# Kernel optimization log

Hardware: AMD Instinct MI355X
Metric: run time of the kernel (lower is better)

The kernel has to match this reference:

```python
import jax, jax.numpy as jnp
from jax import lax
import numpy as np

N = 8000                      # number of input points (also padded unique-voxel count)
PC_RANGE = (-50.0, -50.0, -3.0, 50.0, 50.0, 3.0)
VOXEL = (0.25, 0.25, 6.0)     # cluster_voxel_size
CONN_DIST = 0.6               # connected_dist
GX = int(np.floor((PC_RANGE[3] - PC_RANGE[0]) / VOXEL[0])) + 1
GY = int(np.floor((PC_RANGE[4] - PC_RANGE[1]) / VOXEL[1])) + 1
GZ = int(np.floor((PC_RANGE[5] - PC_RANGE[2]) / VOXEL[2])) + 1


def setup_inputs() -> dict:
    key = jax.random.key(0)
    u = jax.random.uniform(key, (N, 3), dtype=jnp.float32)
    lo = jnp.array(PC_RANGE[:3], jnp.float32)
    hi = jnp.array(PC_RANGE[3:], jnp.float32)
    points = lo + u * (hi - lo)          # points spread over the full pc_range
    batch_idx = jnp.zeros((N,), jnp.int32)  # single batch (eval path)
    return {"points": points, "batch_idx": batch_idx}


def _voxel_ids(points, batch_idx):
    lo = jnp.array(PC_RANGE[:3], dtype=points.dtype)
    vs = jnp.array(VOXEL, dtype=points.dtype)
    coors = jnp.floor((points - lo) / vs).astype(jnp.int32)
    coors = jnp.clip(coors, 0, jnp.array([GX - 1, GY - 1, GZ - 1], jnp.int32))
    # linearize (batch, cx, cy, cz) -> single int id (equivalent to unique over rows)
    return ((batch_idx * GX + coors[:, 0]) * GY + coors[:, 1]) * GZ + coors[:, 2]


def reference(points, batch_idx):
    # ---- scatter_v2(mode='avg'): voxelize + per-voxel mean ----
    vid = _voxel_ids(points, batch_idx)
    _, inv = jnp.unique(vid, size=N, fill_value=-1, return_inverse=True)
    inv = inv.reshape(-1)
    ones = jnp.ones((N,), points.dtype)
    counts = jax.ops.segment_sum(ones, inv, num_segments=N)           # [N]
    centers = jax.ops.segment_sum(points, inv, num_segments=N) / jnp.maximum(counts, 1.0)[:, None]
    valid = counts > 0                                                # real (non-padded) voxels

    # ---- radius adjacency over xy of voxel centers ----
    xy = centers[:, :2]
    sq = jnp.sum(xy * xy, axis=1)
    d2 = sq[:, None] + sq[None, :] - 2.0 * (xy @ xy.T)
    dmat = jnp.sqrt(jnp.maximum(d2, 0.0))                             # [N,N]
    pair_valid = valid[:, None] & valid[None, :]
    adj = (jnp.where(pair_valid, dmat, jnp.inf) < CONN_DIST) | jnp.eye(N, dtype=bool)

    # ---- connected components via min-label propagation + pointer jumping ----
    labels0 = jnp.arange(N, dtype=jnp.int32)

    def body_fn(state):
        l, _ = state
        nl = jnp.min(jnp.where(adj, l[None, :], N), axis=1).astype(jnp.int32)
        nl = jnp.minimum(nl, nl[nl])  # pointer jump accelerates convergence
        return (nl, jnp.all(nl == l))

    labels, _ = lax.while_loop(lambda st: jnp.logical_not(st[1]), body_fn, (labels0, jnp.array(False)))

    # compress component roots to dense 0..K-1 in first-occurrence order
    # (scipy.connected_components labels components by min node index order);
    # padded slots are pushed after all real components.
    comp_key = jnp.where(valid, labels, labels + N)
    _, comp = jnp.unique(comp_key, size=N, fill_value=2 * N, return_inverse=True)
    comp = comp.reshape(-1).astype(jnp.int32)

    cluster_inds = comp[inv]                                          # per-point component id
    cls = jnp.zeros((N,), jnp.int32)                                  # modify_cluster_by_class, class 0
    cluster_inds_per_point = jnp.stack([cls, batch_idx, cluster_inds], axis=1)  # [N,3]
    valid_mask = jnp.ones((N,), bool)                                 # min_points=1 -> all kept
    return cluster_inds_per_point, valid_mask
```

## Files before the change

kernel.cpp:

```cpp
#include <hip/hip_runtime.h>
#include <math.h>
#include <limits.h>

#define NPTS   8000
#define GXD    401
#define GYD    401
#define GZD    2
#define MVOX   321602
#define TS     256
#define NTB    32
#define NPAIR  528

__global__ void k_vid(const float* __restrict__ pts, const int* __restrict__ batch,
                      int* __restrict__ vid, int* __restrict__ V,
                      int* __restrict__ inv, float* __restrict__ cnt,
                      float* __restrict__ sx, float* __restrict__ sy) {
  int p = blockIdx.x * blockDim.x + threadIdx.x;
  if (p >= NPTS) return;
  inv[p] = 0; cnt[p] = 0.0f; sx[p] = 0.0f; sy[p] = 0.0f;
  float x = pts[3 * p + 0], y = pts[3 * p + 1], z = pts[3 * p + 2];
  int cx = (int)floorf((x + 50.0f) / 0.25f);
  int cy = (int)floorf((y + 50.0f) / 0.25f);
  int cz = (int)floorf((z + 3.0f) / 6.0f);
  cx = min(max(cx, 0), GXD - 1);
  cy = min(max(cy, 0), GYD - 1);
  cz = min(max(cz, 0), GZD - 1);
  int b = batch[p];
  int v = ((b * GXD + cx) * GYD + cy) * GZD + cz;
  v = min(max(v, 0), MVOX - 1);
  vid[p] = v;
  atomicMin(&V[v], p);
}

__global__ void k_rank(const int* __restrict__ vid, const int* __restrict__ V,
                       int* __restrict__ inv) {
  __shared__ alignas(16) int rs[TS];
  int t = threadIdx.x;
  int j = blockIdx.y * TS + t;
  int r = INT_MAX;
  if (j < NPTS) {
    int vv = vid[j];
    r = (V[vv] == j) ? vv : INT_MAX;
  }
  rs[t] = r;
  __syncthreads();
  int p = blockIdx.x * TS + t;
  if (p >= NPTS) return;
  int v = vid[p];
  int c = 0;
  const int4* rs4 = (const int4*)rs;
  #pragma unroll 16
  for (int k4 = 0; k4 < TS / 4; ++k4) {
    int4 q = rs4[k4];
    c += (q.x < v) ? 1 : 0;
    c += (q.y < v) ? 1 : 0;
    c += (q.z < v) ? 1 : 0;
    c += (q.w < v) ? 1 : 0;
  }
  if (c) atomicAdd(&inv[p], c);
}

__global__ void k_accum(const float* __restrict__ pts, const int* __restrict__ inv,
                        float* __restrict__ cnt, float* __restrict__ sx,
                        float* __restrict__ sy, int* __restrict__ parent) {
  int p = blockIdx.x * blockDim.x + threadIdx.x;
  if (p >= NPTS) return;
  parent[p] = p;
  int s = inv[p];
  atomicAdd(&cnt[s], 1.0f);
  atomicAdd(&sx[s], pts[3 * p + 0]);
  atomicAdd(&sy[s], pts[3 * p + 1]);
}

__device__ __forceinline__ int load_par(int* parent, int x) {
  return __hip_atomic_load(&parent[x], __ATOMIC_RELAXED, __HIP_MEMORY_SCOPE_AGENT);
}

__device__ void hook(int* parent, int u, int v) {
  int ru = u, rv = v;
  while (true) {
    int p;
    while ((p = load_par(parent, ru)) != ru) ru = p;
    while ((p = load_par(parent, rv)) != rv) rv = p;
    if (ru == rv) return;
    int hi = ru > rv ? ru : rv;
    int lo = ru ^ rv ^ hi;
    int old = atomicCAS(&parent[hi], hi, lo);
    if (old == hi) return;
    ru = lo; rv = old;
  }
}

__device__ __forceinline__ float4 center_of(int u, const float* cnt,
                                            const float* sx, const float* sy) {
  float c = cnt[u];
  float d = fmaxf(c, 1.0f);
  float X = sx[u] / d;
  float Y = sy[u] / d;
  float sq = (c > 0.0f) ? (X * X + Y * Y) : 1e30f;
  return make_float4(X, Y, sq, 0.0f);
}

__global__ void k_edges(const float* __restrict__ cnt, const float* __restrict__ sx,
                        const float* __restrict__ sy, int* __restrict__ parent) {
  __shared__ float4 tile[TS];
  int t = threadIdx.x;
  int e = blockIdx.x;
  int by = (int)((sqrtf(8.0f * (float)e + 1.0f) - 1.0f) * 0.5f);
  while ((by + 1) * (by + 2) / 2 <= e) ++by;
  while (by * (by + 1) / 2 > e) --by;
  int bx = e - by * (by + 1) / 2;
  int j0 = by * TS;
  int j = j0 + t;
  tile[t] = (j < NPTS) ? center_of(j, cnt, sx, sy)
                       : make_float4(0.0f, 0.0f, 1e30f, 0.0f);
  __syncthreads();
  int i = bx * TS + t;
  if (i >= NPTS) return;
  float4 qi = center_of(i, cnt, sx, sy);
  float xi = qi.x, yi = qi.y, si = qi.z;
  for (int kb = 0; kb < TS; kb += 64) {
    unsigned long long m = 0;
    #pragma unroll
    for (int k2 = 0; k2 < 64; ++k2) {
      float4 q = tile[kb + k2];
      float d2 = si + q.z - 2.0f * (xi * q.x + yi * q.y);
      if (d2 < 0.36f) m |= (1ull << k2);
    }
    while (m) {
      int k2 = __ffsll(m) - 1;
      m &= m - 1;
      hook(parent, i, j0 + kb + k2);
    }
  }
}

__global__ void k_post(int* __restrict__ parent, const float* __restrict__ cnt,
                       int* __restrict__ labels, int* __restrict__ compRank) {
  int t = threadIdx.x;
  int b = blockIdx.x;
  if (b == 0) {
    __shared__ int sc[TS];
    unsigned flags = 0;
    int base = t * 32;
    int s = 0;
    #pragma unroll
    for (int k = 0; k < 32; ++k) {
      int i = base + k;
      int fl = 0;
      if (i < NPTS) fl = (cnt[i] > 0.0f && parent[i] == i) ? 1 : 0;
      flags |= (unsigned)fl << k;
      s += fl;
    }
    sc[t] = s;
    __syncthreads();
    for (int off = 1; off < TS; off <<= 1) {
      int v = sc[t];
      int a = (t >= off) ? sc[t - off] : 0;
      __syncthreads();
      sc[t] = v + a;
      __syncthreads();
    }
    int excl = sc[t] - s;
    #pragma unroll
    for (int k = 0; k < 32; ++k) {
      int i = base + k;
      if (i < NPTS) { compRank[i] = excl; excl += (flags >> k) & 1; }
    }
  } else {
    int u = (b - 1) * TS + t;
    if (u < NPTS) {
      int x = u, p;
      while ((p = parent[x]) != x) x = p;
      labels[u] = x;
    }
  }
}

__global__ void k_out(const int* __restrict__ inv, const int* __restrict__ labels,
                      const int* __restrict__ compRank, const int* __restrict__ batch,
                      int* __restrict__ out) {
  int p = blockIdx.x * blockDim.x + threadIdx.x;
  if (p >= NPTS) return;
  int lab = labels[inv[p]];
  out[3 * p + 0] = 0;
  out[3 * p + 1] = batch[p];
  out[3 * p + 2] = compRank[lab];
  out[3 * NPTS + p] = 1;
}

extern "C" void kernel_launch(void* const* d_in, const int* in_sizes, int n_in,
                              void* d_out, int out_size, void* d_ws, size_t ws_size,
                              hipStream_t stream) {
  const float* pts   = (const float*)d_in[0];
  const int*   batch = (const int*)d_in[1];
  int* outp = (int*)d_out;

  char* base = (char*)d_ws;
  size_t o = 0;
  int*   V       = (int*)(base + o);   o += ((size_t)MVOX * 4 + 255) & ~(size_t)255;
  int*   vid     = (int*)(base + o);   o += NPTS * 4;
  int*   inv     = (int*)(base + o);   o += NPTS * 4;
  float* cnt     = (float*)(base + o); o += NPTS * 4;
  float* sx      = (float*)(base + o); o += NPTS * 4;
  float* sy      = (float*)(base + o); o += NPTS * 4;
  int*   parent  = (int*)(base + o);   o += NPTS * 4;
  int*   labels  = (int*)(base + o);   o += NPTS * 4;
  int*   compRank= (int*)(base + o);   o += NPTS * 4;

  hipMemsetAsync(V, 0x7F, (size_t)MVOX * 4, stream);

  dim3 b256(TS);
  k_vid  <<<dim3(NTB),       b256, 0, stream>>>(pts, batch, vid, V, inv, cnt, sx, sy);
  k_rank <<<dim3(NTB, NTB),  b256, 0, stream>>>(vid, V, inv);
  k_accum<<<dim3(NTB),       b256, 0, stream>>>(pts, inv, cnt, sx, sy, parent);
  k_edges<<<dim3(NPAIR),     b256, 0, stream>>>(cnt, sx, sy, parent);
  k_post <<<dim3(NTB + 1),   b256, 0, stream>>>(parent, cnt, labels, compRank);
  k_out  <<<dim3(NTB),       b256, 0, stream>>>(inv, labels, compRank, batch, outp);
}
```

Before: 105.9 us.

## Replace unique/rank pipeline with per-block shared-memory voxel bitmap and fused post-processing

Voxel uniqueness and ranking now come from a shared-memory occupancy bitmap plus a popcount prefix scan, computed redundantly in each of 32 blocks. This removes the 1.3MB memset, the atomicMin table and the O(N^2/256) rank kernel. Each block accumulates the per-voxel sums for its own 250-slot segment in shared memory, so no global atomics are needed. The post and out kernels are merged: each output block recomputes the root-flag scan and finds roots inline. This cuts the launch count from 7 to 3, at the cost of redundant per-block scans and a serial popcount loop over bitmap words for each point.

```diff
diff --git a/kernel.cpp b/kernel.cpp
--- a/kernel.cpp
+++ b/kernel.cpp
@@ -7,17 +7,15 @@
 #define GYD    401
 #define GZD    2
 #define MVOX   321602
+#define NW     10051
+#define NCH    252
 #define TS     256
 #define NTB    32
 #define NPAIR  528
-
-__global__ void k_vid(const float* __restrict__ pts, const int* __restrict__ batch,
-                      int* __restrict__ vid, int* __restrict__ V,
-                      int* __restrict__ inv, float* __restrict__ cnt,
-                      float* __restrict__ sx, float* __restrict__ sy) {
-  int p = blockIdx.x * blockDim.x + threadIdx.x;
-  if (p >= NPTS) return;
-  inv[p] = 0; cnt[p] = 0.0f; sx[p] = 0.0f; sy[p] = 0.0f;
+#define SEGB   250
+
+__device__ __forceinline__ int vox_of(const float* __restrict__ pts,
+                                      const int* __restrict__ batch, int p) {
   float x = pts[3 * p + 0], y = pts[3 * p + 1], z = pts[3 * p + 2];
   int cx = (int)floorf((x + 50.0f) / 0.25f);
   int cy = (int)floorf((y + 50.0f) / 0.25f);
@@ -27,49 +25,63 @@
   cz = min(max(cz, 0), GZD - 1);
   int b = batch[p];
   int v = ((b * GXD + cx) * GYD + cy) * GZD + cz;
-  v = min(max(v, 0), MVOX - 1);
-  vid[p] = v;
-  atomicMin(&V[v], p);
-}
-
-__global__ void k_rank(const int* __restrict__ vid, const int* __restrict__ V,
-                       int* __restrict__ inv) {
-  __shared__ alignas(16) int rs[TS];
-  int t = threadIdx.x;
-  int j = blockIdx.y * TS + t;
-  int r = INT_MAX;
-  if (j < NPTS) {
-    int vv = vid[j];
-    r = (V[vv] == j) ? vv : INT_MAX;
-  }
-  rs[t] = r;
-  __syncthreads();
-  int p = blockIdx.x * TS + t;
-  if (p >= NPTS) return;
-  int v = vid[p];
-  int c = 0;
-  const int4* rs4 = (const int4*)rs;
-  #pragma unroll 16
-  for (int k4 = 0; k4 < TS / 4; ++k4) {
-    int4 q = rs4[k4];
-    c += (q.x < v) ? 1 : 0;
-    c += (q.y < v) ? 1 : 0;
-    c += (q.z < v) ? 1 : 0;
-    c += (q.w < v) ? 1 : 0;
-  }
-  if (c) atomicAdd(&inv[p], c);
-}
-
-__global__ void k_accum(const float* __restrict__ pts, const int* __restrict__ inv,
-                        float* __restrict__ cnt, float* __restrict__ sx,
-                        float* __restrict__ sy, int* __restrict__ parent) {
-  int p = blockIdx.x * blockDim.x + threadIdx.x;
-  if (p >= NPTS) return;
-  parent[p] = p;
-  int s = inv[p];
-  atomicAdd(&cnt[s], 1.0f);
-  atomicAdd(&sx[s], pts[3 * p + 0]);
-  atomicAdd(&sy[s], pts[3 * p + 1]);
+  return min(max(v, 0), MVOX - 1);
+}
+
+__global__ __launch_bounds__(TS) void k_prep(
+    const float* __restrict__ pts, const int* __restrict__ batch,
+    int* __restrict__ inv, float* __restrict__ cnt, float* __restrict__ sx,
+    float* __restrict__ sy, int* __restrict__ parent) {
+  __shared__ unsigned bm[NW];
+  __shared__ int sc[TS];
+  __shared__ int sce[TS];
+  __shared__ float lc[SEGB], lx[SEGB], ly[SEGB];
+  int t = threadIdx.x, b = blockIdx.x;
+
+  for (int w = t; w < NW; w += TS) bm[w] = 0u;
+  if (t < SEGB) { lc[t] = 0.0f; lx[t] = 0.0f; ly[t] = 0.0f; }
+  __syncthreads();
+
+  int vc[32]; int ni = 0;
+  for (int j = t; j < NPTS; j += TS) {
+    int v = vox_of(pts, batch, j);
+    vc[ni++] = v;
+    atomicOr(&bm[v >> 5], 1u << (v & 31));
+  }
+  __syncthreads();
+
+  int s = 0;
+  if (t < NCH) {
+    int w0 = t * 40, w1 = min(NW, w0 + 40);
+    for (int w = w0; w < w1; ++w) s += __popc(bm[w]);
+  }
+  sc[t] = s;
+  __syncthreads();
+  for (int off = 1; off < TS; off <<= 1) {
+    int v = sc[t]; int a = (t >= off) ? sc[t - off] : 0;
+    __syncthreads(); sc[t] = v + a; __syncthreads();
+  }
+  sce[t] = sc[t] - s;
+  __syncthreads();
+
+  int s0 = b * SEGB;
+  ni = 0;
+  for (int j = t; j < NPTS; j += TS) {
+    int v = vc[ni++];
+    int w = v >> 5, c0 = w / 40;
+    int r = sce[c0];
+    for (int ww = c0 * 40; ww < w; ++ww) r += __popc(bm[ww]);
+    r += __popc(bm[w] & ((1u << (v & 31)) - 1u));
+    int lr = r - s0;
+    if (lr >= 0 && lr < SEGB) {
+      atomicAdd(&lc[lr], 1.0f);
+      atomicAdd(&lx[lr], pts[3 * j + 0]);
+      atomicAdd(&ly[lr], pts[3 * j + 1]);
+    }
+    if (j >= s0 && j < s0 + SEGB) { inv[j] = r; parent[j] = j; }
+  }
+  __syncthreads();
+  if (t < SEGB) { int u = s0 + t; cnt[u] = lc[t]; sx[u] = lx[t]; sy[u] = ly[t]; }
 }
 
 __device__ __forceinline__ int load_par(int* parent, int x) {
@@ -135,57 +147,42 @@
   }
 }
 
-__global__ void k_post(int* __restrict__ parent, const float* __restrict__ cnt,
-                       int* __restrict__ labels, int* __restrict__ compRank) {
-  int t = threadIdx.x;
-  int b = blockIdx.x;
-  if (b == 0) {
-    __shared__ int sc[TS];
-    unsigned flags = 0;
-    int base = t * 32;
-    int s = 0;
-    #pragma unroll
+__global__ __launch_bounds__(TS) void k_outw(
+    const int* __restrict__ inv, int* __restrict__ parent,
+    const float* __restrict__ cnt, const int* __restrict__ batch,
+    int* __restrict__ out) {
+  __shared__ unsigned fw[SEGB];
+  __shared__ int sc[TS];
+  __shared__ int wex[TS];
+  int t = threadIdx.x, b = blockIdx.x;
+  int s = 0;
+  if (t < SEGB) {
+    unsigned wword = 0;
+    int i0 = t * 32;
     for (int k = 0; k < 32; ++k) {
-      int i = base + k;
-      int fl = 0;
-      if (i < NPTS) fl = (cnt[i] > 0.0f && parent[i] == i) ? 1 : 0;
-      flags |= (unsigned)fl << k;
-      s += fl;
-    }
-    sc[t] = s;
-    __syncthreads();
-    for (int off = 1; off < TS; off <<= 1) {
-      int v = sc[t];
-      int a = (t >= off) ? sc[t - off] : 0;
-      __syncthreads();
-      sc[t] = v + a;
-      __syncthreads();
-    }
-    int excl = sc[t] - s;
-    #pragma unroll
-    for (int k = 0; k < 32; ++k) {
-      int i = base + k;
-      if (i < NPTS) { compRank[i] = excl; excl += (flags >> k) & 1; }
-    }
-  } else {
-    int u = (b - 1) * TS + t;
-    if (u < NPTS) {
-      int x = u, p;
-      while ((p = parent[x]) != x) x = p;
-      labels[u] = x;
-    }
-  }
-}
-
-__global__ void k_out(const int* __restrict__ inv, const int* __restrict__ labels,
-                      const int* __restrict__ compRank, const int* __restrict__ batch,
-                      int* __restrict__ out) {
-  int p = blockIdx.x * blockDim.x + threadIdx.x;
+      int i = i0 + k;
+      int fl = (cnt[i] > 0.0f && parent[i] == i) ? 1 : 0;
+      wword |= (unsigned)fl << k;
+    }
+    fw[t] = wword;
+    s = __popc(wword);
+  }
+  sc[t] = s;
+  __syncthreads();
+  for (int off = 1; off < TS; off <<= 1) {
+    int v = sc[t]; int a = (t >= off) ? sc[t - off] : 0;
+    __syncthreads(); sc[t] = v + a; __syncthreads();
+  }
+  wex[t] = sc[t] - s;
+  __syncthreads();
+  int p = b * TS + t;
   if (p >= NPTS) return;
-  int lab = labels[inv[p]];
+  int x = inv[p], q;
+  while ((q = parent[x]) != x) x = q;
+  int c = wex[x >> 5] + __popc(fw[x >> 5] & ((1u << (x & 31)) - 1u));
   out[3 * p + 0] = 0;
   out[3 * p + 1] = batch[p];
-  out[3 * p + 2] = compRank[lab];
+  out[3 * p + 2] = c;
   out[3 * NPTS + p] = 1;
 }
 
@@ -198,23 +195,14 @@
 
   char* base = (char*)d_ws;
   size_t o = 0;
-  int*   V       = (int*)(base + o);   o += ((size_t)MVOX * 4 + 255) & ~(size_t)255;
-  int*   vid     = (int*)(base + o);   o += NPTS * 4;
   int*   inv     = (int*)(base + o);   o += NPTS * 4;
   float* cnt     = (float*)(base + o); o += NPTS * 4;
   float* sx      = (float*)(base + o); o += NPTS * 4;
   float* sy      = (float*)(base + o); o += NPTS * 4;
   int*   parent  = (int*)(base + o);   o += NPTS * 4;
-  int*   labels  = (int*)(base + o);   o += NPTS * 4;
-  int*   compRank= (int*)(base + o);   o += NPTS * 4;
-
-  hipMemsetAsync(V, 0x7F, (size_t)MVOX * 4, stream);
 
   dim3 b256(TS);
-  k_vid  <<<dim3(NTB),       b256, 0, stream>>>(pts, batch, vid, V, inv, cnt, sx, sy);
-  k_rank <<<dim3(NTB, NTB),  b256, 0, stream>>>(vid, V, inv);
-  k_accum<<<dim3(NTB),       b256, 0, stream>>>(pts, inv, cnt, sx, sy, parent);
-  k_edges<<<dim3(NPAIR),     b256, 0, stream>>>(cnt, sx, sy, parent);
-  k_post <<<dim3(NTB + 1),   b256, 0, stream>>>(parent, cnt, labels, compRank);
-  k_out  <<<dim3(NTB),       b256, 0, stream>>>(inv, labels, compRank, batch, outp);
-}
+  k_prep <<<dim3(NTB),   b256, 0, stream>>>(pts, batch, inv, cnt, sx, sy, parent);
+  k_edges<<<dim3(NPAIR), b256, 0, stream>>>(cnt, sx, sy, parent);
+  k_outw <<<dim3(NTB),   b256, 0, stream>>>(inv, parent, cnt, batch, outp);
+}
```

Result: slower. 133.8 us (+26.3%).
